# Kernel optimization log

Hardware: AMD Instinct MI355X
Metric: run time of the kernel (lower is better)

## Reference

```python
import jax, jax.numpy as jnp
import numpy as np

S_DIM = 4096
N_NODES = 4096
N_EDGES = 32768


def _coarsen(ei_np, N):
    """Integer-only greedy coarsening, faithful to MNGRAPH.forward's while-loop.
    Returns (select order, flattened neighbor indices, segment ids, per-hub
    neighbor counts, forward-fill indices replicating the stale-M behavior for
    empty neighborhoods, and the remapped final edge_index)."""
    ei = ei_np.astype(np.int64).copy()
    I = np.bincount(ei[0], minlength=N)
    O = np.bincount(ei[1], minlength=N)
    order = np.argsort(-(I + O), kind='stable')  # torch.argsort(D, descending=True)
    visits = np.zeros(N, dtype=bool)
    select = []
    nbr_idx, nbr_seg, counts = [], [], []
    while order.size > 0:
        node = int(order[0])
        select.append(node)
        visits[node] = True
        # H = unique neighbors of node in the CURRENT (rewritten) edge_index
        H = np.unique(np.concatenate([ei[1][ei[0] == node], ei[0][ei[1] == node]]))
        visits[H] = True
        order = order[~visits[order]]
        # rewrite: endpoints in H that are not already-selected hubs -> node
        Hn = H[~np.isin(H, np.asarray(select, dtype=np.int64))]
        ei[np.isin(ei, Hn)] = node
        ei = ei[:, ei[0] != ei[1]]  # drop self-loops
        # append reversed edges that are not already present (pair-code isin
        # == the original O(E^2) all/any comparison, computed efficiently)
        code = ei[0] * N + ei[1]
        rcode = ei[1] * N + ei[0]
        new = ~np.isin(rcode, code)
        ei = np.concatenate([ei, ei[::-1][:, new]], axis=1)
        k = len(select) - 1
        nbr_idx.append(H)
        nbr_seg.append(np.full(H.shape[0], k, dtype=np.int64))
        counts.append(H.shape[0])
    select = np.asarray(select, dtype=np.int64)
    sort_sel = np.sort(select)
    ei_out = np.searchsorted(sort_sel, ei)  # compact node ids
    counts = np.asarray(counts, dtype=np.int64)
    # forward-fill: when H is empty the original appends the previous (stale) M
    fill = np.arange(select.shape[0])
    for i in range(select.shape[0]):
        if counts[i] == 0:
            fill[i] = fill[i - 1] if i > 0 else 0
    nbr = np.concatenate(nbr_idx) if nbr_idx else np.zeros(0, np.int64)
    seg = np.concatenate(nbr_seg) if nbr_seg else np.zeros(0, np.int64)
    return select, nbr, seg, counts, fill, ei_out


def setup_inputs() -> dict:
    key = jax.random.key(0)
    k1, k2, k3, k4 = jax.random.split(key, 4)
    x = jax.random.normal(k1, (N_NODES, S_DIM), dtype=jnp.float32)
    edge_index = jax.random.randint(k2, (2, N_EDGES), 0, N_NODES, dtype=jnp.int64)
    bound = float(np.sqrt(6.0 / (1.0 + S_DIM)))  # xavier_uniform on (1, S)
    W1 = jax.random.uniform(k3, (S_DIM,), jnp.float32, -bound, bound)
    W2 = jax.random.uniform(k4, (S_DIM,), jnp.float32, -bound, bound)
    B1 = jnp.zeros((S_DIM,), jnp.float32)
    B2 = jnp.zeros((S_DIM,), jnp.float32)
    return {"x": x, "edge_index": edge_index, "W1": W1, "W2": W2, "B1": B1, "B2": B2}


def reference(x, edge_index, W1, W2, B1, B2):
    N = x.shape[0]
    sel, nbr, seg, counts, fill, ei_out = _coarsen(np.asarray(edge_index), N)
    K = sel.shape[0]
    # Dn = x[n]*W1+B1 for every neighbor of every hub; per-hub mean via segment_sum
    Dn = x[jnp.asarray(nbr)] * W1 + B1                      # [T, S]
    sums = jax.ops.segment_sum(Dn, jnp.asarray(seg), num_segments=K)
    denom = jnp.maximum(jnp.asarray(counts), 1).astype(x.dtype)[:, None]
    mean_Dn = sums / denom                                  # [K, S]
    Dv = x[jnp.asarray(sel)] * W2 + B2                      # [K, S]
    END = jnp.concatenate([Dv, mean_Dn], axis=1)            # [K, 2S]
    END = END[jnp.asarray(fill)]                            # stale-M replication
    return END, jnp.asarray(ei_out)
```

## Files before the change

### kernel.cpp

```cpp
#include <hip/hip_runtime.h>
#include <hip/hip_bf16.h>

#define NT 1024
#define NNODES 4096
#define ECAP 65536

__global__ __launch_bounds__(256)
void zeroBM(int4* __restrict__ bm) {
    bm[(size_t)blockIdx.x * 256 + threadIdx.x] = make_int4(0, 0, 0, 0);
}

__device__ __forceinline__ int blockScanExcl(int v, int* s_w, int* total) {
    const int tid  = threadIdx.x;
    const int lane = tid & 63;
    const int wv   = tid >> 6;
    int x = v;
#pragma unroll
    for (int off = 1; off < 64; off <<= 1) {
        int t = __shfl_up(x, off, 64);
        if (lane >= off) x += t;
    }
    if (lane == 63) s_w[wv] = x;
    __syncthreads();
    if (tid < 16) {
        int y = s_w[tid];
#pragma unroll
        for (int off = 1; off < 16; off <<= 1) {
            int t = __shfl_up(y, off, 16);
            if (tid >= off) y += t;
        }
        s_w[tid] = y;
    }
    __syncthreads();
    int base = wv ? s_w[wv - 1] : 0;
    int tot  = s_w[15];
    __syncthreads();
    *total = tot;
    return base + x - v;
}

__global__ __launch_bounds__(NT, 1)
void phaseA1(const int* __restrict__ ei, int E0,
             int* __restrict__ U, int* __restrict__ V,
             unsigned int* __restrict__ BM,
             int* __restrict__ NBR, int* __restrict__ OTH,
             int* __restrict__ ORDV, int* __restrict__ ROFFG, int* __restrict__ RENDG,
             int* __restrict__ HAND)
{
    __shared__ unsigned short s_order[NNODES];
    __shared__ unsigned char  s_vis[NNODES];
    __shared__ unsigned char  s_rank[NNODES];
    __shared__ unsigned int   s_hb[NNODES / 32];
    __shared__ int s_roff[NNODES];
    __shared__ int s_rend[NNODES];
    __shared__ int s_tmp[NNODES];
    __shared__ int s_mat[64][65];
    __shared__ int s_w[16];
    __shared__ int s_bc[16];

    const int tid = threadIdx.x;

    for (int i = tid; i < NNODES; i += NT) { s_vis[i] = 0; s_tmp[i] = 0; }
    for (int i = tid; i < NNODES / 32; i += NT) s_hb[i] = 0;
    if (tid < 16) s_bc[tid] = 0;
    __syncthreads();

    for (int i = tid; i < E0; i += NT)
        if (ei[2 * i + 1] != 0) s_bc[9] = 1;
    __syncthreads();
    const int is64 = !s_bc[9];

    for (int e = tid; e < E0; e += NT) {
        int uu = ei[is64 ? 2 * e : e];
        int vv = ei[is64 ? 2 * (E0 + e) : (E0 + e)];
        U[e] = uu; V[e] = vv;
        atomicAdd(&s_tmp[uu], 1);
        atomicAdd(&s_tmp[vv], 1);
    }
    __syncthreads();
    for (int n = tid; n < NNODES; n += NT) atomicMax(&s_bc[7], s_tmp[n]);
    __syncthreads();
    const int maxd = s_bc[7];

    if (maxd < 64) {
        const int wv = tid >> 6, lane = tid & 63;
        const unsigned long long ltm = (1ull << lane) - 1ull;
        for (int g = wv; g < 64; g += 16) {
            int n = g * 64 + lane;
            int d = s_tmp[n];
            int rk = 0;
            for (int dd = 0; dd < 64; ++dd) {
                unsigned long long bal = __ballot(d == dd);
                if (lane == 0) s_mat[dd][g] = __popcll(bal);
                if (d == dd) rk = __popcll(bal & ltm);
            }
            s_rank[n] = (unsigned char)rk;
        }
        __syncthreads();
        if (tid < 64) {
            int run = 0;
            for (int g = 0; g < 64; ++g) { int t = s_mat[tid][g]; s_mat[tid][g] = run; run += t; }
            s_mat[tid][64] = run;
        }
        __syncthreads();
        if (tid < 64) {
            int x = s_mat[tid][64];
#pragma unroll
            for (int off = 1; off < 64; off <<= 1) {
                int t = __shfl_up(x, off, 64);
                if (tid >= off) x += t;
            }
            int T = __shfl(x, 63, 64);
            s_mat[tid][64] = T - x;
        }
        __syncthreads();
        for (int g = wv; g < 64; g += 16) {
            int n = g * 64 + lane;
            int d = s_tmp[n];
            int pos = s_mat[d][64] + s_mat[d][g] + (int)s_rank[n];
            s_order[pos] = (unsigned short)n;
        }
        __syncthreads();
    } else {
        for (int d = maxd; d >= 0; --d) {
            int n0 = tid * 4;
            int f0 = (s_tmp[n0] == d), f1 = (s_tmp[n0 + 1] == d);
            int f2 = (s_tmp[n0 + 2] == d), f3 = (s_tmp[n0 + 3] == d);
            int tot;
            int off = blockScanExcl(f0 + f1 + f2 + f3, s_w, &tot);
            int idx = s_bc[4] + off;
            if (f0) s_order[idx++] = (unsigned short)n0;
            if (f1) s_order[idx++] = (unsigned short)(n0 + 1);
            if (f2) s_order[idx++] = (unsigned short)(n0 + 2);
            if (f3) s_order[idx++] = (unsigned short)(n0 + 3);
            __syncthreads();
            if (tid == 0) s_bc[4] += tot;
            __syncthreads();
        }
    }

    if (tid == 0) {
        int nd = s_order[0];
        s_bc[0] = nd; s_vis[nd] = 1;
    }
    __syncthreads();
    {
        const int node = s_bc[0];
        for (int e = tid; e < E0; e += NT) {
            int uu = U[e], vv = V[e];
            if (uu == node) {
                int w = vv; unsigned m = 1u << (w & 31);
                unsigned old = atomicOr(&s_hb[w >> 5], m);
                if (!(old & m)) { int i = atomicAdd(&s_bc[2], 1); s_tmp[i] = w; s_vis[w] = 1; }
            }
            if (vv == node) {
                int w = uu; unsigned m = 1u << (w & 31);
                unsigned old = atomicOr(&s_hb[w >> 5], m);
                if (!(old & m)) { int i = atomicAdd(&s_bc[2], 1); s_tmp[i] = w; s_vis[w] = 1; }
            }
        }
        __syncthreads();
        for (int e = tid; e < E0; e += NT) {
            int uu = U[e];
            if (uu != node && ((s_hb[uu >> 5] >> (uu & 31)) & 1)) U[e] = node;
            int vv = V[e];
            if (vv != node && ((s_hb[vv >> 5] >> (vv & 31)) & 1)) V[e] = node;
        }
        __syncthreads();
    }

    for (int e = tid; e < E0; e += NT) {
        int uu = U[e], vv = V[e];
        if (uu != vv) {
            unsigned code = ((unsigned)uu << 12) | (unsigned)vv;
            atomicOr(&BM[code >> 5], 1u << (code & 31));
        }
    }
    __syncthreads();
    for (int t0 = 0; t0 < E0; t0 += NT * 32) {
        unsigned fm = 0u;
        const int base = t0 + tid * 32;
        for (int j = 0; j < 32; ++j) {
            int e = base + j;
            if (e < E0) {
                int uu = U[e], vv = V[e];
                if (uu != vv) {
                    unsigned rc = ((unsigned)vv << 12) | (unsigned)uu;
                    unsigned old = atomicOr(&BM[rc >> 5], 0u);
                    if (!((old >> (rc & 31)) & 1u)) fm |= (1u << j);
                }
            }
        }
        int tot;
        int off = blockScanExcl(__popc(fm), s_w, &tot);
        int r = s_bc[5] + off;
        unsigned m = fm;
        while (m) {
            int j = __ffs((int)m) - 1; m &= m - 1;
            int e = base + j;
            U[E0 + r] = V[e]; V[E0 + r] = U[e];
            ++r;
        }
        __syncthreads();
        if (tid == 0) s_bc[5] += tot;
        __syncthreads();
    }
    const int E1 = E0 + s_bc[5];

    for (int n = tid; n < NNODES; n += NT) s_roff[n] = 0;
    __syncthreads();
    for (int e = tid; e < E1; e += NT) {
        int uu = U[e], vv = V[e];
        if (uu != vv) atomicAdd(&s_roff[uu], 1);
    }
    __syncthreads();
    {
        int n0 = tid * 4;
        int c0 = s_roff[n0], c1 = s_roff[n0 + 1], c2 = s_roff[n0 + 2], c3 = s_roff[n0 + 3];
        int tot;
        int off = blockScanExcl(c0 + c1 + c2 + c3, s_w, &tot);
        int st = off;
        s_roff[n0] = st;     s_rend[n0] = st;     st += c0;
        s_roff[n0 + 1] = st; s_rend[n0 + 1] = st; st += c1;
        s_roff[n0 + 2] = st; s_rend[n0 + 2] = st; st += c2;
        s_roff[n0 + 3] = st; s_rend[n0 + 3] = st;
    }
    __syncthreads();
    for (int e = tid; e < E1; e += NT) {
        int uu = U[e], vv = V[e];
        if (uu != vv) {
            int p = atomicAdd(&s_rend[uu], 1);
            OTH[p] = vv;
        }
    }
    __syncthreads();
    {
        const int cnt0 = s_bc[2];
        for (int i = tid; i < cnt0; i += NT) NBR[i] = s_tmp[i];
    }
    for (int i = tid; i < NNODES; i += NT) {
        int nd = (int)s_order[i];
        ORDV[i]  = nd | (s_vis[nd] ? 0x8000 : 0);
        ROFFG[i] = s_roff[i];
        RENDG[i] = s_rend[i];
    }
    if (tid == 0) { HAND[0] = E1; HAND[1] = s_bc[2]; HAND[2] = s_bc[0]; }
}

__global__ __launch_bounds__(64, 1)
void phaseA2(const int* __restrict__ OTH, int* __restrict__ NBR,
             const int* __restrict__ ORDV, const int* __restrict__ ROFFG,
             const int* __restrict__ RENDG, const int* __restrict__ HAND,
             int* __restrict__ SEL, int* __restrict__ CNTS,
             int* __restrict__ NST, int* __restrict__ FIL, int* __restrict__ SC,
             int* __restrict__ LABG, int* __restrict__ RNKG)
{
    __shared__ unsigned short s_ord[NNODES];
    __shared__ unsigned int   s_visbits[NNODES / 32];
    __shared__ unsigned int   s_meta[NNODES];
    __shared__ unsigned short s_so[NNODES];
    __shared__ int s_cnt[NNODES];
    __shared__ int s_stamp[NNODES];
    __shared__ int s_roff[NNODES];
    __shared__ int s_rend[NNODES];

    const int ln = threadIdx.x;
    const unsigned long long ltm = (1ull << ln) - 1ull;
    const int cnt0 = HAND[1], hub0 = HAND[2];
    volatile int* vstamp = s_stamp;

    for (int i = ln; i < NNODES / 32; i += 64) s_visbits[i] = 0u;
    for (int i = ln; i < NNODES; i += 64) {
        int ov = ORDV[i];
        int nd = ov & 0x7FFF;
        s_ord[i] = (unsigned short)nd;
        s_meta[nd] = ((unsigned)i << 16) | (unsigned)nd;
        s_roff[i] = ROFFG[i];
        s_rend[i] = RENDG[i];
        s_stamp[i] = 0; s_cnt[i] = 0;
        if (ov & 0x8000) atomicOr(&s_visbits[i >> 5], 1u << (i & 31));
    }
    if (ln == 0) {
        s_meta[hub0] = (unsigned)hub0 | 0x8000u;
        s_so[0] = (unsigned short)hub0;
        s_cnt[0] = cnt0;
    }

    int nc = cnt0;
    int k = 1;

    unsigned lo = 0u, hi = 0u;
    auto extract = [&]() -> int {
        unsigned long long b = __ballot(lo != 0u);
        if (b) {
            int sl = __ffsll((long long)b) - 1;
            unsigned ww = __shfl(lo, sl, 64);
            if (ln == sl) lo &= lo - 1;
            return sl * 32 + (__ffs((int)ww) - 1);
        }
        b = __ballot(hi != 0u);
        if (b) {
            int sl = __ffsll((long long)b) - 1;
            unsigned ww = __shfl(hi, sl, 64);
            if (ln == sl) hi &= hi - 1;
            return 2048 + sl * 32 + (__ffs((int)ww) - 1);
        }
        return -1;
    };

    auto commitNew = [&](unsigned g, int w, bool nw, unsigned long long bal,
                         unsigned relv) {
        if (nw) {
            NBR[nc + __popcll(bal & ltm)] = w;
            int slot = (int)(g >> 16);
            atomicOr(&s_visbits[slot >> 5], 1u << (slot & 31));
            if (!(g & 0x8000u)) s_meta[w] = relv;
        }
        nc += __popcll(bal);
    };

    auto procFast = [&](int hub, int hslot, int o, unsigned g) {
        const unsigned relv = ((unsigned)hslot << 16) | (unsigned)hub | 0x8000u;
        int w = (o >= 0) ? (int)(g & 0x7FFFu) : hub;
        bool valid = (o >= 0) && (w != hub);
        if (valid) vstamp[w] = ln;
        int r = valid ? vstamp[w] : -1;
        bool nw = valid && (r == ln);
        unsigned long long bal = __ballot(nw);
        commitNew(g, w, nw, bal, relv);
    };

    auto procSlow = [&](int hub, int hslot, int rb, int re, int o0) {
        const unsigned relv = ((unsigned)hslot << 16) | (unsigned)hub | 0x8000u;
        const int key = k << 6;
        int o = o0;
        for (int s0 = rb; s0 < re; s0 += 64) {
            unsigned g = (o >= 0) ? s_meta[o] : 0u;
            int w = (o >= 0) ? (int)(g & 0x7FFFu) : hub;
            bool cnd = (w != hub);
            int old = key;
            if (cnd) old = atomicMax(&s_stamp[w], key);
            bool nw = cnd && (old < key);
            unsigned long long bal = __ballot(nw);
            commitNew(g, w, nw, bal, relv);
            int s1 = s0 + 64;
            o = (s1 + ln < re) ? OTH[s1 + ln] : -1;
        }
    };

    int nsl0=-1,nsl1=-1,nsl2=-1,nsl3=-1,nsl4=-1,nsl5=-1,nsl6=-1,nsl7=-1;
    int ncd0=-1,ncd1=-1,ncd2=-1,ncd3=-1,ncd4=-1,ncd5=-1,ncd6=-1,ncd7=-1;
    int nrb0=0,nrb1=0,nrb2=0,nrb3=0,nrb4=0,nrb5=0,nrb6=0,nrb7=0;
    int nre0=0,nre1=0,nre2=0,nre3=0,nre4=0,nre5=0,nre6=0,nre7=0;
    int nv0=-1,nv1=-1,nv2=-1,nv3=-1,nv4=-1,nv5=-1,nv6=-1,nv7=-1;

#define PF_ONE(i) \
    ncd##i = (nsl##i >= 0) ? (int)s_ord[nsl##i] : -1; \
    nrb##i = 0; nre##i = 0; \
    if (ncd##i >= 0) { nrb##i = s_roff[ncd##i]; nre##i = s_rend[ncd##i]; } \
    nv##i = (ncd##i >= 0 && nrb##i + ln < nre##i) ? OTH[nrb##i + ln] : -1;

#define PREFETCH_OCTET() do { \
    lo = ~s_visbits[ln]; hi = ~s_visbits[ln + 64]; \
    nsl0 = extract(); nsl1 = extract(); nsl2 = extract(); nsl3 = extract(); \
    nsl4 = extract(); nsl5 = extract(); nsl6 = extract(); nsl7 = extract(); \
    { int ms = (ln==0)?nsl0:(ln==1)?nsl1:(ln==2)?nsl2:(ln==3)?nsl3: \
               (ln==4)?nsl4:(ln==5)?nsl5:(ln==6)?nsl6:nsl7; \
      if (ln < 8 && ms >= 0) atomicOr(&s_visbits[ms >> 5], 1u << (ms & 31)); } \
    PF_ONE(0) PF_ONE(1) PF_ONE(2) PF_ONE(3) PF_ONE(4) PF_ONE(5) PF_ONE(6) PF_ONE(7) \
} while (0)

#define DO_CAND(CC, SLI, RBI, REI, VI) \
    if (CC >= 0) { \
        unsigned mm = s_meta[CC]; \
        unsigned gg = (VI >= 0) ? s_meta[VI] : 0u; \
        if ((int)(mm & 0x7FFFu) == CC) { \
            if (ln == 0) { \
                s_meta[CC] = ((unsigned)SLI << 16) | (unsigned)CC | 0x8000u; \
                s_so[k] = (unsigned short)CC; \
            } \
            int begin = nc; \
            if (REI - RBI <= 64) procFast(CC, SLI, VI, gg); \
            else                 procSlow(CC, SLI, RBI, REI, VI); \
            if (ln == 0) s_cnt[k] = nc - begin; \
            k++; \
        } \
    }

    PREFETCH_OCTET();
    for (;;) {
        int c0=ncd0,c1=ncd1,c2=ncd2,c3=ncd3,c4=ncd4,c5=ncd5,c6=ncd6,c7=ncd7;
        int t0=nsl0,t1=nsl1,t2=nsl2,t3=nsl3,t4=nsl4,t5=nsl5,t6=nsl6,t7=nsl7;
        int a0=nrb0,a1=nrb1,a2=nrb2,a3=nrb3,a4=nrb4,a5=nrb5,a6=nrb6,a7=nrb7;
        int e0=nre0,e1=nre1,e2=nre2,e3=nre3,e4=nre4,e5=nre5,e6=nre6,e7=nre7;
        int v0=nv0,v1=nv1,v2=nv2,v3=nv3,v4=nv4,v5=nv5,v6=nv6,v7=nv7;
        if (c0 < 0) break;
        PREFETCH_OCTET();
        DO_CAND(c0, t0, a0, e0, v0);
        DO_CAND(c1, t1, a1, e1, v1);
        DO_CAND(c2, t2, a2, e2, v2);
        DO_CAND(c3, t3, a3, e3, v3);
        DO_CAND(c4, t4, a4, e4, v4);
        DO_CAND(c5, t5, a5, e5, v5);
        DO_CAND(c6, t6, a6, e6, v6);
        DO_CAND(c7, t7, a7, e7, v7);
    }
#undef DO_CAND
#undef PREFETCH_OCTET
#undef PF_ONE
    const int K = k;

    {
        int base = 0;
        for (int c = 0; c < NNODES / 64; ++c) {
            int n = c * 64 + ln;
            unsigned mv = s_meta[n];
            int f = ((mv & 0x8000u) != 0u) && ((int)(mv & 0x7FFFu) == n);
            unsigned long long b = __ballot(f);
            s_stamp[n] = base + __popcll(b & ltm);
            base += __popcll(b);
        }
    }
    {
        int nb = 0;
        for (int c = 0; c * 64 < K; ++c) {
            int i = c * 64 + ln;
            int cv = (i < K) ? s_cnt[i] : 0;
            int x = cv;
#pragma unroll
            for (int off = 1; off < 64; off <<= 1) {
                int t = __shfl_up(x, off, 64);
                if (ln >= off) x += t;
            }
            if (i < K) { NST[i] = nb + x - cv; CNTS[i] = cv; SEL[i] = (int)s_so[i]; }
            nb += __shfl(x, 63, 64);
        }
    }
    {
        int carry = 0;
        for (int c = 0; c * 64 < K; ++c) {
            int i = c * 64 + ln;
            int f = (i < K) && (s_cnt[i] > 0);
            unsigned long long b = __ballot(f);
            unsigned long long m = b & ((ln == 63) ? ~0ull : ((1ull << (ln + 1)) - 1ull));
            int fil = m ? (c * 64 + 63 - __clzll(m)) : carry;
            if (i < K) FIL[i] = fil;
            carry = b ? (c * 64 + 63 - __clzll(b)) : carry;
        }
    }
    if (ln == 0) SC[0] = K;
    for (int i = ln; i < NNODES; i += 64) {
        LABG[i] = (int)(s_meta[i] & 0x7FFFu);
        RNKG[i] = s_stamp[i];
    }
}

__global__ __launch_bounds__(NT, 1)
void phaseA3(const int* __restrict__ U, const int* __restrict__ V,
             const int* __restrict__ LABG, const int* __restrict__ RNKG,
             const int* __restrict__ HAND, int* __restrict__ SC,
             int* __restrict__ TMP, float* __restrict__ out)
{
    __shared__ unsigned short l_lab[NNODES];
    __shared__ int l_rnk[NNODES];
    __shared__ int s_w[16];
    __shared__ int s_base[1];

    const int tid = threadIdx.x;
    for (int i = tid; i < NNODES; i += NT) {
        l_lab[i] = (unsigned short)LABG[i];
        l_rnk[i] = RNKG[i];
    }
    if (tid == 0) s_base[0] = 0;
    __syncthreads();

    const int E1 = HAND[0];
    const int K  = SC[0];
    const size_t obase = (size_t)K * 8192;

    for (int t0 = 0; t0 < E1; t0 += NT * 64) {
        unsigned long long fm = 0ull;
        const int base = t0 + tid * 64;
        if (base + 64 <= E1) {
            const int4* U4 = (const int4*)(U + base);
            const int4* V4 = (const int4*)(V + base);
#pragma unroll
            for (int q = 0; q < 16; ++q) {
                int4 a = U4[q], b = V4[q];
                int j = q * 4;
                if ((int)l_lab[a.x] != (int)l_lab[b.x]) fm |= 1ull << j;
                if ((int)l_lab[a.y] != (int)l_lab[b.y]) fm |= 1ull << (j + 1);
                if ((int)l_lab[a.z] != (int)l_lab[b.z]) fm |= 1ull << (j + 2);
                if ((int)l_lab[a.w] != (int)l_lab[b.w]) fm |= 1ull << (j + 3);
            }
        } else {
            for (int j = 0; j < 64; ++j) {
                int e = base + j;
                if (e < E1) {
                    if ((int)l_lab[U[e]] != (int)l_lab[V[e]]) fm |= 1ull << j;
                }
            }
        }
        int tot;
        int off = blockScanExcl(__popcll(fm), s_w, &tot);
        int r = s_base[0] + off;
        unsigned long long m = fm;
        while (m) {
            int j = __ffsll((long long)m) - 1; m &= m - 1;
            int e = base + j;
            out[obase + (size_t)r] = (float)l_rnk[(int)l_lab[U[e]]];
            TMP[r] = l_rnk[(int)l_lab[V[e]]];
            ++r;
        }
        __syncthreads();
        if (tid == 0) s_base[0] += tot;
        __syncthreads();
    }
    const int Ef = s_base[0];
    if (tid == 0) SC[1] = Ef;
    for (int r = tid; r < Ef; r += NT)
        out[obase + (size_t)Ef + (size_t)r] = (float)TMP[r];
}

__global__ __launch_bounds__(256, 4)
void phaseB(const float* __restrict__ x,
            const float* __restrict__ W1, const float* __restrict__ W2,
            const float* __restrict__ B1, const float* __restrict__ B2,
            const int* __restrict__ NBR, const int* __restrict__ SEL,
            const int* __restrict__ CNTS, const int* __restrict__ NST,
            const int* __restrict__ FIL, const int* __restrict__ SC,
            float* __restrict__ out)
{
    const int K = SC[0];
    const int k = blockIdx.x;
    if (k >= K) return;
    const int kk   = FIL[k];
    const int node = SEL[kk];
    const int cnt  = CNTS[kk];
    const int st   = NST[kk];
    const int tid  = threadIdx.x;
    const float4* x4 = (const float4*)x;

    float4 acc[4];
#pragma unroll
    for (int j = 0; j < 4; j++) acc[j] = make_float4(0.f, 0.f, 0.f, 0.f);

    for (int r = 0; r < cnt; ++r) {
        const float4* row = x4 + (size_t)NBR[st + r] * 1024;
#pragma unroll
        for (int j = 0; j < 4; j++) {
            float4 t = row[tid + j * 256];
            acc[j].x += t.x; acc[j].y += t.y; acc[j].z += t.z; acc[j].w += t.w;
        }
    }

    const float fc  = (float)cnt;
    const float inv = 1.0f / (float)(cnt > 1 ? cnt : 1);
    const float4* xr = x4 + (size_t)node * 1024;
    float4* o4 = (float4*)(out + (size_t)k * 8192);

#pragma unroll
    for (int j = 0; j < 4; j++) {
        int c = tid + j * 256;
        float4 w1 = ((const float4*)W1)[c], b1 = ((const float4*)B1)[c];
        float4 w2 = ((const float4*)W2)[c], b2 = ((const float4*)B2)[c];
        float4 xv = xr[c];
        float4 pd, pm;
        pd.x = xv.x * w2.x + b2.x;
        pd.y = xv.y * w2.y + b2.y;
        pd.z = xv.z * w2.z + b2.z;
        pd.w = xv.w * w2.w + b2.w;
        pm.x = (acc[j].x * w1.x + fc * b1.x) * inv;
        pm.y = (acc[j].y * w1.y + fc * b1.y) * inv;
        pm.z = (acc[j].z * w1.z + fc * b1.z) * inv;
        pm.w = (acc[j].w * w1.w + fc * b1.w) * inv;
        o4[c] = pd;
        o4[1024 + c] = pm;
    }
}

extern "C" void kernel_launch(void* const* d_in, const int* in_sizes, int n_in,
                              void* d_out, int out_size, void* d_ws, size_t ws_size,
                              hipStream_t stream)
{
    const float* x  = (const float*)d_in[0];
    const int*   ei = (const int*)d_in[1];
    const float* W1 = (const float*)d_in[2];
    const float* W2 = (const float*)d_in[3];
    const float* B1 = (const float*)d_in[4];
    const float* B2 = (const float*)d_in[5];
    const int E0 = in_sizes[1] / 2;

    char* w = (char*)d_ws;
    int* U = (int*)w;
    int* V = U + ECAP;
    unsigned int* BM = (unsigned int*)(V + ECAP);
    int* OTH = (int*)BM;
    int* NBR = OTH + 2 * ECAP;
    int* TMP = NBR + 2 * ECAP;
    char* meta = (char*)BM + (2u << 20);
    int* SEL   = (int*)meta;
    int* CNTS  = SEL  + NNODES;
    int* NST   = CNTS + NNODES;
    int* FIL   = NST  + NNODES;
    int* SC    = FIL  + NNODES;
    int* ORDV  = SC   + 16;
    int* ROFFG = ORDV + NNODES;
    int* RENDG = ROFFG + NNODES;
    int* LABG  = RENDG + NNODES;
    int* RNKG  = LABG + NNODES;
    int* HAND  = RNKG + NNODES;
    float* out = (float*)d_out;

    hipLaunchKernelGGL(zeroBM, dim3(512), dim3(256), 0, stream, (int4*)BM);

    hipLaunchKernelGGL(phaseA1, dim3(1), dim3(NT), 0, stream,
                       ei, E0, U, V, BM, NBR, OTH, ORDV, ROFFG, RENDG, HAND);
    hipLaunchKernelGGL(phaseA2, dim3(1), dim3(64), 0, stream,
                       OTH, NBR, ORDV, ROFFG, RENDG, HAND,
                       SEL, CNTS, NST, FIL, SC, LABG, RNKG);
    hipLaunchKernelGGL(phaseA3, dim3(1), dim3(NT), 0, stream,
                       U, V, LABG, RNKG, HAND, SC, TMP, out);
    hipLaunchKernelGGL(phaseB, dim3(NNODES), dim3(256), 0, stream,
                       x, W1, W2, B1, B2, NBR, SEL, CNTS, NST, FIL, SC, out);
}
```

Baseline: 1.043 ms.

## Process two small-degree hub candidates per wavefront using half-wave lanes

Restructures the serial greedy coarsening loop so that two consecutive candidate hubs with at most 32 neighbors each are handled together, one per half of the 64-lane wavefront. A conflict check (lanes claiming across halves, or hub A touching hub B) falls back to sequential solo processing, which keeps the results identical. It also removes the cross-iteration software prefetch of the next octet and loads neighbor lists just in time. The aim is to halve the per-hub serial steps for low-degree nodes. In exchange it adds extra ballots and branch overhead, and the loads are no longer overlapped with work.

Result: faster. 1.012 ms (-2.9%).

```diff
diff --git a/kernel.cpp b/kernel.cpp
--- a/kernel.cpp
+++ b/kernel.cpp
@@ -266,6 +266,8 @@
 
     const int ln = threadIdx.x;
     const unsigned long long ltm = (1ull << ln) - 1ull;
+    const int half  = ln >> 5;
+    const int hlane = ln & 31;
     const int cnt0 = HAND[1], hub0 = HAND[2];
     volatile int* vstamp = s_stamp;
 
@@ -308,106 +310,143 @@
         return -1;
     };
 
-    auto commitNew = [&](unsigned g, int w, bool nw, unsigned long long bal,
-                         unsigned relv) {
+    auto soloHalf = [&](int C, int S, int HALF, int PV) {
+        const unsigned relv = ((unsigned)S << 16) | (unsigned)C | 0x8000u;
+        if (ln == 0) s_meta[C] = relv;
+        bool lv = (PV >= 0) && (half == HALF);
+        unsigned g = lv ? s_meta[PV] : 0u;
+        int w = lv ? (int)(g & 0x7FFFu) : C;
+        bool cnd = lv && (w != C);
+        if (cnd) vstamp[w] = ln;
+        int r = cnd ? vstamp[w] : -1;
+        bool nw = cnd && (r == ln);
+        unsigned long long bal = __ballot(nw);
         if (nw) {
             NBR[nc + __popcll(bal & ltm)] = w;
             int slot = (int)(g >> 16);
             atomicOr(&s_visbits[slot >> 5], 1u << (slot & 31));
             if (!(g & 0x8000u)) s_meta[w] = relv;
         }
-        nc += __popcll(bal);
+        int cnt = (int)__popcll(bal);
+        if (ln == 0) { s_so[k] = (unsigned short)C; s_cnt[k] = cnt; }
+        nc += cnt; k++;
     };
 
-    auto procFast = [&](int hub, int hslot, int o, unsigned g) {
-        const unsigned relv = ((unsigned)hslot << 16) | (unsigned)hub | 0x8000u;
-        int w = (o >= 0) ? (int)(g & 0x7FFFu) : hub;
-        bool valid = (o >= 0) && (w != hub);
-        if (valid) vstamp[w] = ln;
-        int r = valid ? vstamp[w] : -1;
-        bool nw = valid && (r == ln);
-        unsigned long long bal = __ballot(nw);
-        commitNew(g, w, nw, bal, relv);
-    };
-
-    auto procSlow = [&](int hub, int hslot, int rb, int re, int o0) {
-        const unsigned relv = ((unsigned)hslot << 16) | (unsigned)hub | 0x8000u;
+    auto soloFull = [&](int C, int S, int RB, int RE) {
+        const unsigned relv = ((unsigned)S << 16) | (unsigned)C | 0x8000u;
+        if (ln == 0) s_meta[C] = relv;
         const int key = k << 6;
-        int o = o0;
-        for (int s0 = rb; s0 < re; s0 += 64) {
+        int begin = nc;
+        for (int s0 = RB; s0 < RE; s0 += 64) {
+            int o = (s0 + ln < RE) ? OTH[s0 + ln] : -1;
             unsigned g = (o >= 0) ? s_meta[o] : 0u;
-            int w = (o >= 0) ? (int)(g & 0x7FFFu) : hub;
-            bool cnd = (w != hub);
+            int w = (o >= 0) ? (int)(g & 0x7FFFu) : C;
+            bool cnd = (w != C);
             int old = key;
             if (cnd) old = atomicMax(&s_stamp[w], key);
             bool nw = cnd && (old < key);
             unsigned long long bal = __ballot(nw);
-            commitNew(g, w, nw, bal, relv);
-            int s1 = s0 + 64;
-            o = (s1 + ln < re) ? OTH[s1 + ln] : -1;
-        }
+            if (nw) {
+                NBR[nc + __popcll(bal & ltm)] = w;
+                int slot = (int)(g >> 16);
+                atomicOr(&s_visbits[slot >> 5], 1u << (slot & 31));
+                if (!(g & 0x8000u)) s_meta[w] = relv;
+            }
+            nc += (int)__popcll(bal);
+        }
+        if (ln == 0) { s_so[k] = (unsigned short)C; s_cnt[k] = nc - begin; }
+        k++;
     };
 
-    int nsl0=-1,nsl1=-1,nsl2=-1,nsl3=-1,nsl4=-1,nsl5=-1,nsl6=-1,nsl7=-1;
-    int ncd0=-1,ncd1=-1,ncd2=-1,ncd3=-1,ncd4=-1,ncd5=-1,ncd6=-1,ncd7=-1;
-    int nrb0=0,nrb1=0,nrb2=0,nrb3=0,nrb4=0,nrb5=0,nrb6=0,nrb7=0;
-    int nre0=0,nre1=0,nre2=0,nre3=0,nre4=0,nre5=0,nre6=0,nre7=0;
-    int nv0=-1,nv1=-1,nv2=-1,nv3=-1,nv4=-1,nv5=-1,nv6=-1,nv7=-1;
-
-#define PF_ONE(i) \
-    ncd##i = (nsl##i >= 0) ? (int)s_ord[nsl##i] : -1; \
-    nrb##i = 0; nre##i = 0; \
-    if (ncd##i >= 0) { nrb##i = s_roff[ncd##i]; nre##i = s_rend[ncd##i]; } \
-    nv##i = (ncd##i >= 0 && nrb##i + ln < nre##i) ? OTH[nrb##i + ln] : -1;
-
-#define PREFETCH_OCTET() do { \
-    lo = ~s_visbits[ln]; hi = ~s_visbits[ln + 64]; \
-    nsl0 = extract(); nsl1 = extract(); nsl2 = extract(); nsl3 = extract(); \
-    nsl4 = extract(); nsl5 = extract(); nsl6 = extract(); nsl7 = extract(); \
-    { int ms = (ln==0)?nsl0:(ln==1)?nsl1:(ln==2)?nsl2:(ln==3)?nsl3: \
-               (ln==4)?nsl4:(ln==5)?nsl5:(ln==6)?nsl6:nsl7; \
-      if (ln < 8 && ms >= 0) atomicOr(&s_visbits[ms >> 5], 1u << (ms & 31)); } \
-    PF_ONE(0) PF_ONE(1) PF_ONE(2) PF_ONE(3) PF_ONE(4) PF_ONE(5) PF_ONE(6) PF_ONE(7) \
-} while (0)
-
-#define DO_CAND(CC, SLI, RBI, REI, VI) \
-    if (CC >= 0) { \
-        unsigned mm = s_meta[CC]; \
-        unsigned gg = (VI >= 0) ? s_meta[VI] : 0u; \
-        if ((int)(mm & 0x7FFFu) == CC) { \
-            if (ln == 0) { \
-                s_meta[CC] = ((unsigned)SLI << 16) | (unsigned)CC | 0x8000u; \
-                s_so[k] = (unsigned short)CC; \
-            } \
-            int begin = nc; \
-            if (REI - RBI <= 64) procFast(CC, SLI, VI, gg); \
-            else                 procSlow(CC, SLI, RBI, REI, VI); \
-            if (ln == 0) s_cnt[k] = nc - begin; \
-            k++; \
-        } \
-    }
-
-    PREFETCH_OCTET();
+    auto doPair = [&](int CA, int SA, int RBA, int REA,
+                      int CB, int SB, int RBB, int REB, int PV) {
+        if (CA < 0 && CB < 0) return;
+        bool okA = (CA >= 0) && ((int)(s_meta[CA] & 0x7FFFu) == CA);
+        bool okB = (CB >= 0) && ((int)(s_meta[CB] & 0x7FFFu) == CB);
+        int lenA = (CA >= 0) ? (REA - RBA) : 0;
+        int lenB = (CB >= 0) ? (REB - RBB) : 0;
+        if (okA && okB && lenA <= 32 && lenB <= 32) {
+            const unsigned relvA = ((unsigned)SA << 16) | (unsigned)CA | 0x8000u;
+            const unsigned relvB = ((unsigned)SB << 16) | (unsigned)CB | 0x8000u;
+            if (ln == 0) s_meta[CA] = relvA;
+            unsigned g = (PV >= 0) ? s_meta[PV] : 0u;
+            int hub = (half == 0) ? CA : CB;
+            int w = (PV >= 0) ? (int)(g & 0x7FFFu) : hub;
+            bool valid = (PV >= 0) && (w != hub);
+            if (valid) vstamp[w] = ln;
+            int r = valid ? vstamp[w] : -1;
+            bool bad = (valid && (((r ^ ln) & 32) != 0)) ||
+                       (valid && half == 0 && w == CB);
+            if (__ballot(bad) == 0ull) {
+                bool nw = valid && (r == ln);
+                unsigned long long bal = __ballot(nw);
+                if (nw) {
+                    NBR[nc + __popcll(bal & ltm)] = w;
+                    int slot = (int)(g >> 16);
+                    atomicOr(&s_visbits[slot >> 5], 1u << (slot & 31));
+                    unsigned relv = (half == 0) ? relvA : relvB;
+                    if (!(g & 0x8000u)) s_meta[w] = relv;
+                }
+                int cA = (int)__popcll(bal & 0xFFFFFFFFull);
+                int cB = (int)__popcll(bal >> 32);
+                if (ln == 0) {
+                    s_meta[CB] = relvB;
+                    s_so[k] = (unsigned short)CA;     s_cnt[k] = cA;
+                    s_so[k + 1] = (unsigned short)CB; s_cnt[k + 1] = cB;
+                }
+                nc += cA + cB; k += 2;
+                return;
+            }
+            soloHalf(CA, SA, 0, PV);
+            if ((int)(s_meta[CB] & 0x7FFFu) == CB) soloHalf(CB, SB, 1, PV);
+            return;
+        }
+        if (okA) {
+            if (lenA <= 32) soloHalf(CA, SA, 0, PV);
+            else            soloFull(CA, SA, RBA, REA);
+        }
+        if (CB >= 0 && (int)(s_meta[CB] & 0x7FFFu) == CB) {
+            if (lenB <= 32) soloHalf(CB, SB, 1, PV);
+            else            soloFull(CB, SB, RBB, REB);
+        }
+    };
+
     for (;;) {
-        int c0=ncd0,c1=ncd1,c2=ncd2,c3=ncd3,c4=ncd4,c5=ncd5,c6=ncd6,c7=ncd7;
-        int t0=nsl0,t1=nsl1,t2=nsl2,t3=nsl3,t4=nsl4,t5=nsl5,t6=nsl6,t7=nsl7;
-        int a0=nrb0,a1=nrb1,a2=nrb2,a3=nrb3,a4=nrb4,a5=nrb5,a6=nrb6,a7=nrb7;
-        int e0=nre0,e1=nre1,e2=nre2,e3=nre3,e4=nre4,e5=nre5,e6=nre6,e7=nre7;
-        int v0=nv0,v1=nv1,v2=nv2,v3=nv3,v4=nv4,v5=nv5,v6=nv6,v7=nv7;
-        if (c0 < 0) break;
-        PREFETCH_OCTET();
-        DO_CAND(c0, t0, a0, e0, v0);
-        DO_CAND(c1, t1, a1, e1, v1);
-        DO_CAND(c2, t2, a2, e2, v2);
-        DO_CAND(c3, t3, a3, e3, v3);
-        DO_CAND(c4, t4, a4, e4, v4);
-        DO_CAND(c5, t5, a5, e5, v5);
-        DO_CAND(c6, t6, a6, e6, v6);
-        DO_CAND(c7, t7, a7, e7, v7);
-    }
-#undef DO_CAND
-#undef PREFETCH_OCTET
-#undef PF_ONE
+        lo = ~s_visbits[ln]; hi = ~s_visbits[ln + 64];
+        int sl0 = extract(); int sl1 = extract(); int sl2 = extract(); int sl3 = extract();
+        int sl4 = extract(); int sl5 = extract(); int sl6 = extract(); int sl7 = extract();
+        if (sl0 < 0) break;
+        {
+            int ms = (ln==0)?sl0:(ln==1)?sl1:(ln==2)?sl2:(ln==3)?sl3:
+                     (ln==4)?sl4:(ln==5)?sl5:(ln==6)?sl6:sl7;
+            if (ln < 8 && ms >= 0) atomicOr(&s_visbits[ms >> 5], 1u << (ms & 31));
+        }
+        int c0 = (sl0>=0)?(int)s_ord[sl0]:-1; int c1 = (sl1>=0)?(int)s_ord[sl1]:-1;
+        int c2 = (sl2>=0)?(int)s_ord[sl2]:-1; int c3 = (sl3>=0)?(int)s_ord[sl3]:-1;
+        int c4 = (sl4>=0)?(int)s_ord[sl4]:-1; int c5 = (sl5>=0)?(int)s_ord[sl5]:-1;
+        int c6 = (sl6>=0)?(int)s_ord[sl6]:-1; int c7 = (sl7>=0)?(int)s_ord[sl7]:-1;
+
+        int rb0=0,re0=0,rb1=0,re1=0,rb2=0,re2=0,rb3=0,re3=0;
+        int rb4=0,re4=0,rb5=0,re5=0,rb6=0,re6=0,rb7=0,re7=0;
+        if (c0>=0){rb0=s_roff[c0];re0=s_rend[c0];} if (c1>=0){rb1=s_roff[c1];re1=s_rend[c1];}
+        if (c2>=0){rb2=s_roff[c2];re2=s_rend[c2];} if (c3>=0){rb3=s_roff[c3];re3=s_rend[c3];}
+        if (c4>=0){rb4=s_roff[c4];re4=s_rend[c4];} if (c5>=0){rb5=s_roff[c5];re5=s_rend[c5];}
+        if (c6>=0){rb6=s_roff[c6];re6=s_rend[c6];} if (c7>=0){rb7=s_roff[c7];re7=s_rend[c7];}
+
+        int b0 = (half==0)?rb0:rb1, l0 = (half==0)?re0:re1; bool k0 = (half==0)?(c0>=0):(c1>=0);
+        int b1 = (half==0)?rb2:rb3, l1 = (half==0)?re2:re3; bool k1 = (half==0)?(c2>=0):(c3>=0);
+        int b2 = (half==0)?rb4:rb5, l2 = (half==0)?re4:re5; bool k2 = (half==0)?(c4>=0):(c5>=0);
+        int b3 = (half==0)?rb6:rb7, l3 = (half==0)?re6:re7; bool k3 = (half==0)?(c6>=0):(c7>=0);
+        int pv0 = (k0 && b0 + hlane < l0) ? OTH[b0 + hlane] : -1;
+        int pv1 = (k1 && b1 + hlane < l1) ? OTH[b1 + hlane] : -1;
+        int pv2 = (k2 && b2 + hlane < l2) ? OTH[b2 + hlane] : -1;
+        int pv3 = (k3 && b3 + hlane < l3) ? OTH[b3 + hlane] : -1;
+
+        doPair(c0, sl0, rb0, re0, c1, sl1, rb1, re1, pv0);
+        doPair(c2, sl2, rb2, re2, c3, sl3, rb3, re3, pv1);
+        doPair(c4, sl4, rb4, re4, c5, sl5, rb5, re5, pv2);
+        doPair(c6, sl6, rb6, re6, c7, sl7, rb7, re7, pv3);
+    }
     const int K = k;
 
     {
```
